# Kernel optimization log

Hardware: AMD Instinct MI355X
Metric: run time of the kernel (lower is better)

## Reference

```python
import jax, jax.numpy as jnp
import numpy as np
from jax import lax

INV_SQRT2 = np.float32(1.0 / np.sqrt(2.0))

def conv2d(x, w, b=None, stride=1, pad=0):
    y = lax.conv_general_dilated(x, w, (stride, stride), [(pad, pad), (pad, pad)],
                                 dimension_numbers=('NCHW', 'OIHW', 'NCHW'))
    return y if b is None else y + b[None, :, None, None]

def haar_dwt2_zero(x):
    # pytorch_wavelets DWTForward(J=1, wave='haar', mode='zero') for odd H,W:
    # pad one zero at the end of each spatial dim, then pairwise Haar analysis.
    x = jnp.pad(x, ((0, 0), (0, 0), (0, 1), (0, 1)))
    xe, xo = x[..., 0::2], x[..., 1::2]
    lo_w, hi_w = (xe + xo) * INV_SQRT2, (xe - xo) * INV_SQRT2
    def rows(t):
        te, to = t[:, :, 0::2, :], t[:, :, 1::2, :]
        return (te + to) * INV_SQRT2, (te - to) * INV_SQRT2
    ll, lh = rows(lo_w)
    hl, hh = rows(hi_w)
    return ll, lh, hl, hh  # cA, cH, cV, cD

def pixel_shuffle2(x):
    B, C, H, W = x.shape
    co = C // 4
    return x.reshape(B, co, 2, 2, H, W).transpose(0, 1, 4, 2, 5, 3).reshape(B, co, H * 2, W * 2)

def gaussian_kernel5(sigma=0.5):
    r = np.arange(5, dtype=np.float64) - 2.0
    k = np.exp(-(r ** 2) / (2.0 * sigma * sigma))
    return jnp.asarray((k / k.sum()).astype(np.float32))

_GK = gaussian_kernel5(0.5)

def gaussian_blur5(x4d):
    # cv2.GaussianBlur ksize=(5,5) sigma=0.5, default BORDER_REFLECT_101 -> 'reflect' pad
    p = jnp.pad(x4d, ((0, 0), (0, 0), (2, 2), (2, 2)), mode='reflect')
    p = conv2d(p, _GK.reshape(1, 1, 5, 1))
    return conv2d(p, _GK.reshape(1, 1, 1, 5))

def channel_attention(x, w1, w2):
    avg = jnp.mean(x, axis=(2, 3), keepdims=True)
    mx = jnp.max(x, axis=(2, 3), keepdims=True)
    mlp = lambda v: conv2d(jax.nn.relu(conv2d(v, w1)), w2)
    return jax.nn.sigmoid(mlp(avg) + mlp(mx)) * x

def _forward(x, w_x1, b_x1, w_x2, b_x2, w_x3, b_x3, w_hi, b_hi, w_lo, b_lo,
             ca1_w1, ca1_w2, ca2_w1, ca2_w2, w_cat, b_cat, w_c9a, b_c9a, w_c9b, b_c9b):
    f1 = jax.nn.relu(conv2d(x, w_x1, b_x1))            # (1,16,H,W)
    f2 = jax.nn.relu(conv2d(f1, w_x2, b_x2))           # (1,8,H,W)
    tmp12 = jax.nn.relu(conv2d(f2, w_x3, b_x3))        # (1,1,H,W)
    cA, cH, cV, cD = haar_dwt2_zero(tmp12)             # each (1,1,(H+1)/2,(W+1)/2)
    hf = pixel_shuffle2(jax.nn.relu(conv2d(jnp.concatenate([cH, cV, cD], 1), w_hi, b_hi, pad=1)))
    lf = pixel_shuffle2(jax.nn.relu(conv2d(cA, w_lo, b_lo, pad=1)))  # (1,1,H+5,W+5)
    # original detaches hf (cpu->numpy->cv2->cuda): gradients do not flow through it
    hf = gaussian_blur5(lax.stop_gradient(hf))
    hf = channel_attention(hf, ca1_w1, ca1_w2)
    lf = channel_attention(lf, ca2_w1, ca2_w2)
    alpha = 1.0
    cat = jax.nn.relu(conv2d(jnp.concatenate([alpha * hf, (1.0 - alpha) * lf], 1), w_cat, b_cat))
    f12 = tmp12 + cat                                   # (1,1,H,W)
    h = jax.nn.relu(conv2d(f12, w_c9a, b_c9a, pad=1))   # (1,32,H,W)
    return jax.nn.relu(conv2d(h, w_c9b, b_c9b, pad=1))  # (1,64,H,W)

def setup_inputs() -> dict:
    key = jax.random.key(0)
    ks = jax.random.split(key, 24)
    f32 = jnp.float32
    n = lambda k, s, sc=0.05: jax.random.normal(k, s, f32) * sc
    H = W = 511
    return {
        'x': jax.random.normal(ks[0], (1, 204, H, W), f32),
        'w_x1': n(ks[1], (16, 204, 1, 1)), 'b_x1': n(ks[2], (16,)),
        'w_x2': n(ks[3], (8, 16, 1, 1)),   'b_x2': n(ks[4], (8,)),
        'w_x3': n(ks[5], (1, 8, 1, 1)),    'b_x3': n(ks[6], (1,)),
        'w_hi': n(ks[7], (4, 3, 1, 1)),    'b_hi': n(ks[8], (4,)),
        'w_lo': n(ks[9], (4, 1, 1, 1)),    'b_lo': n(ks[10], (4,)),
        'ca1_w1': n(ks[11], (1, 1, 1, 1), 0.5), 'ca1_w2': n(ks[12], (1, 1, 1, 1), 0.5),
        'ca2_w1': n(ks[13], (1, 1, 1, 1), 0.5), 'ca2_w2': n(ks[14], (1, 1, 1, 1), 0.5),
        'w_cat': n(ks[15], (1, 2, 6, 6)),  'b_cat': n(ks[16], (1,)),
        'w_c9a': n(ks[17], (32, 1, 3, 3)), 'b_c9a': n(ks[18], (32,)),
        'w_c9b': n(ks[19], (64, 32, 3, 3)), 'b_c9b': n(ks[20], (64,)),
    }

def reference(x, w_x1, b_x1, w_x2, b_x2, w_x3, b_x3, w_hi, b_hi, w_lo, b_lo,
              ca1_w1, ca1_w2, ca2_w1, ca2_w2, w_cat, b_cat, w_c9a, b_c9a, w_c9b, b_c9b):
    return _forward(x, w_x1, b_x1, w_x2, b_x2, w_x3, b_x3, w_hi, b_hi, w_lo, b_lo,
                    ca1_w1, ca1_w2, ca2_w1, ca2_w2, w_cat, b_cat, w_c9a, b_c9a, w_c9b, b_c9b)
```

## Files before the change

### kernel.cpp

```cpp
#include <hip/hip_runtime.h>
#include <math.h>

#define NP    261121
#define HALF  130561
#define WPX   520
#define ROWN  4160
#define PSTR  2138240
#define NBLUR 1041

typedef __attribute__((ext_vector_type(8))) short short8;
typedef __attribute__((ext_vector_type(4))) float f32x4;

static __device__ __forceinline__ unsigned short f2bf(float f) {
    unsigned int u = __builtin_bit_cast(unsigned int, f);
    u += 0x7FFFu + ((u >> 16) & 1u);
    return (unsigned short)(u >> 16);
}

__global__ __launch_bounds__(256) void k_prep(const float* __restrict__ w_c9a,
                                              const float* __restrict__ w_c9b,
                                              const float* __restrict__ w_x1,
                                              float* __restrict__ wTa,
                                              unsigned short* __restrict__ wb2,
                                              float* __restrict__ wT1,
                                              unsigned short* __restrict__ h2)
{
    int t = blockIdx.x * 256 + threadIdx.x;
    if (t < 288)  wTa[t] = w_c9a[(t & 31) * 9 + (t >> 5)];
    if (t < 3264) wT1[t] = w_x1[(t & 15) * 204 + (t >> 4)];
    if (t < 18432) {
        int o = t / 288, ck = t - o * 288;
        int c = ck / 9, k = ck - c * 9;
        wb2[k * 2048 + o * 32 + c] = f2bf(w_c9b[t]);
    }
    short8 z8 = {0, 0, 0, 0, 0, 0, 0, 0};
    if (t < 4160) {
        int pl = t / 1040;
        int rr = t - pl * 1040;
        int row = rr >= 520 ? 512 : 0;
        int ch  = rr >= 520 ? rr - 520 : rr;
        *reinterpret_cast<short8*>(h2 + (size_t)pl * PSTR + (size_t)row * ROWN + ch * 8) = z8;
    }
    int z = t - 4160;
    if (z >= 0 && z < 6132) {
        int row = z / 12 + 1;
        int j = z - (row - 1) * 12;
        int pl = j / 3, cidx = j - pl * 3;
        int col = (cidx == 0) ? 0 : (cidx == 1 ? 512 : 513);
        *reinterpret_cast<short8*>(h2 + (size_t)pl * PSTR + (size_t)row * ROWN + col * 8) = z8;
    }
}

__global__ __launch_bounds__(512) void k_conv123(const float* __restrict__ x,
                                                 const float* __restrict__ wT1,
                                                 const float* __restrict__ b1,
                                                 const float* __restrict__ w2,
                                                 const float* __restrict__ b2,
                                                 const float* __restrict__ w3,
                                                 const float* __restrict__ b3,
                                                 float* __restrict__ tmp12)
{
    __shared__ float sw[3264];
    int t = threadIdx.x;
    for (int i = t; i < 3264; i += 512) sw[i] = wT1[i];
    __syncthreads();

    int g = blockIdx.x * 512 + t;
    if (g >= HALF) return;
    int p0 = g, p1 = g + HALF;
    bool has1 = p1 < NP;
    int p1c = has1 ? p1 : p0;

    float acc0[16], acc1[16];
#pragma unroll
    for (int o = 0; o < 16; ++o) { acc0[o] = 0.f; acc1[o] = 0.f; }

#pragma unroll 4
    for (int c = 0; c < 204; ++c) {
        float xv0 = x[c * NP + p0];
        float xv1 = x[c * NP + p1c];
        const float4* wv = reinterpret_cast<const float4*>(sw + c * 16);
        float wl[16];
        *reinterpret_cast<float4*>(&wl[0])  = wv[0];
        *reinterpret_cast<float4*>(&wl[4])  = wv[1];
        *reinterpret_cast<float4*>(&wl[8])  = wv[2];
        *reinterpret_cast<float4*>(&wl[12]) = wv[3];
#pragma unroll
        for (int o = 0; o < 16; ++o) {
            acc0[o] = fmaf(xv0, wl[o], acc0[o]);
            acc1[o] = fmaf(xv1, wl[o], acc1[o]);
        }
    }

    float r0 = b3[0], r1 = b3[0];
    {
        float f10[16], f11[16];
#pragma unroll
        for (int o = 0; o < 16; ++o) {
            float bo = b1[o];
            f10[o] = fmaxf(acc0[o] + bo, 0.f);
            f11[o] = fmaxf(acc1[o] + bo, 0.f);
        }
#pragma unroll
        for (int j = 0; j < 8; ++j) {
            float s0 = b2[j], s1 = b2[j];
#pragma unroll
            for (int o = 0; o < 16; ++o) {
                float w = w2[j * 16 + o];
                s0 = fmaf(f10[o], w, s0);
                s1 = fmaf(f11[o], w, s1);
            }
            float wj = w3[j];
            r0 = fmaf(fmaxf(s0, 0.f), wj, r0);
            r1 = fmaf(fmaxf(s1, 0.f), wj, r1);
        }
    }
    tmp12[p0] = fmaxf(r0, 0.f);
    if (has1) tmp12[p1] = fmaxf(r1, 0.f);
}

__global__ __launch_bounds__(256) void k_dwt_hi(const float* __restrict__ tmp12,
                                                const float* __restrict__ w_hi,
                                                const float* __restrict__ b_hi,
                                                float* __restrict__ hf)
{
    const float INV = 0.70710678118654752440f;
    int idx = blockIdx.x * 256 + threadIdx.x;
    if (idx >= 258 * 258) return;
    int h = idx / 258, w = idx - h * 258;

    float wh[12], bh[4];
#pragma unroll
    for (int i = 0; i < 12; ++i) wh[i] = w_hi[i];
#pragma unroll
    for (int o = 0; o < 4; ++o) bh[o] = b_hi[o];

    float v[4];
    if (h == 0 || h == 257 || w == 0 || w == 257) {
#pragma unroll
        for (int o = 0; o < 4; ++o) v[o] = fmaxf(bh[o], 0.f);
    } else {
        int hh = h - 1, ww = w - 1;
        int r0 = 2 * hh, r1 = 2 * hh + 1, c0 = 2 * ww, c1 = 2 * ww + 1;
        float a = tmp12[r0 * 511 + c0];
        float b = (c1 < 511) ? tmp12[r0 * 511 + c1] : 0.f;
        float c = (r1 < 511) ? tmp12[r1 * 511 + c0] : 0.f;
        float d = (r1 < 511 && c1 < 511) ? tmp12[r1 * 511 + c1] : 0.f;
        float lo0 = (a + b) * INV, hi0 = (a - b) * INV;
        float lo1 = (c + d) * INV, hi1 = (c - d) * INV;
        float cH = (lo0 - lo1) * INV;
        float cV = (hi0 + hi1) * INV;
        float cD = (hi0 - hi1) * INV;
#pragma unroll
        for (int o = 0; o < 4; ++o)
            v[o] = fmaxf(wh[o * 3 + 0] * cH + wh[o * 3 + 1] * cV + wh[o * 3 + 2] * cD + bh[o], 0.f);
    }
    int orow = (2 * h) * 516 + 2 * w;
    hf[orow]       = v[0];
    hf[orow + 1]   = v[1];
    hf[orow + 516] = v[2];
    hf[orow + 517] = v[3];
}

__global__ __launch_bounds__(256) void k_blur(const float* __restrict__ hf,
                                              float* __restrict__ hfb,
                                              float* __restrict__ psum,
                                              float* __restrict__ pmax,
                                              float g0, float g1, float g2)
{
    __shared__ float ss[256], sm[256];
    int t = threadIdx.x;
    int idx = blockIdx.x * 256 + t;
    bool ok = idx < 516 * 516;
    int idc = ok ? idx : 0;
    int y = idc / 516, x = idc - y * 516;
    float g[5] = {g0, g1, g2, g1, g0};
    int ry[5], rx[5];
#pragma unroll
    for (int i = 0; i < 5; ++i) {
        int yy = y + i - 2; yy = yy < 0 ? -yy : (yy > 515 ? 1030 - yy : yy);
        int xx = x + i - 2; xx = xx < 0 ? -xx : (xx > 515 ? 1030 - xx : xx);
        ry[i] = yy * 516; rx[i] = xx;
    }
    float s = 0.f;
#pragma unroll
    for (int i = 0; i < 5; ++i) {
        float rs = 0.f;
#pragma unroll
        for (int j = 0; j < 5; ++j) rs = fmaf(g[j], hf[ry[i] + rx[j]], rs);
        s = fmaf(g[i], rs, s);
    }
    if (ok) hfb[idx] = s;

    ss[t] = ok ? s : 0.f;
    sm[t] = ok ? s : -3.4e38f;
    __syncthreads();
    for (int off = 128; off > 0; off >>= 1) {
        if (t < off) { ss[t] += ss[t + off]; sm[t] = fmaxf(sm[t], sm[t + off]); }
        __syncthreads();
    }
    if (t == 0) { psum[blockIdx.x] = ss[0]; pmax[blockIdx.x] = sm[0]; }
}

__global__ __launch_bounds__(256) void k_cat(const float* __restrict__ hfb,
                                             const float* __restrict__ tmp12,
                                             const float* __restrict__ psum,
                                             const float* __restrict__ pmax,
                                             const float* __restrict__ caw1,
                                             const float* __restrict__ caw2,
                                             const float* __restrict__ w_cat,
                                             const float* __restrict__ b_cat,
                                             float* __restrict__ f12)
{
    __shared__ float ss[256], sm[256], ssc;
    int t = threadIdx.x;
    {
        float s = 0.f, m = -3.4e38f;
        for (int i = t; i < NBLUR; i += 256) { s += psum[i]; m = fmaxf(m, pmax[i]); }
        ss[t] = s; sm[t] = m;
        __syncthreads();
        for (int off = 128; off > 0; off >>= 1) {
            if (t < off) { ss[t] += ss[t + off]; sm[t] = fmaxf(sm[t], sm[t + off]); }
            __syncthreads();
        }
        if (t == 0) {
            float avg = ss[0] / 266256.f;
            float a = caw1[0], b = caw2[0];
            float z = b * fmaxf(a * avg, 0.f) + b * fmaxf(a * sm[0], 0.f);
            ssc = 1.f / (1.f + expf(-z));
        }
        __syncthreads();
    }
    float sc = ssc;

    int p = blockIdx.x * 256 + t;
    if (p >= NP) return;
    int y = p / 511, x = p - y * 511;
    float s = 0.f;
#pragma unroll
    for (int ky = 0; ky < 6; ++ky) {
        const float* row = hfb + (y + ky) * 516 + x;
#pragma unroll
        for (int kx = 0; kx < 6; ++kx) s = fmaf(row[kx], w_cat[ky * 6 + kx], s);
    }
    f12[p] = tmp12[p] + fmaxf(sc * s + b_cat[0], 0.f);
}

__global__ __launch_bounds__(256) void k_c9a(const float* __restrict__ f12,
                                             const float* __restrict__ wTa,
                                             const float* __restrict__ bias,
                                             unsigned short* __restrict__ h2)
{
    int p = blockIdx.x * 256 + threadIdx.x;
    if (p >= NP) return;
    int y = p / 511, x = p - y * 511;
    float hv[9];
#pragma unroll
    for (int ky = 0; ky < 3; ++ky)
#pragma unroll
        for (int kx = 0; kx < 3; ++kx) {
            int yy = y + ky - 1, xx = x + kx - 1;
            hv[ky * 3 + kx] = (yy >= 0 && yy < 511 && xx >= 0 && xx < 511) ? f12[yy * 511 + xx] : 0.f;
        }
    float acc[32];
#pragma unroll
    for (int o = 0; o < 32; ++o) acc[o] = bias[o];
#pragma unroll
    for (int k = 0; k < 9; ++k) {
        float v = hv[k];
        const float* wp = wTa + k * 32;
#pragma unroll
        for (int o = 0; o < 32; ++o) acc[o] = fmaf(v, wp[o], acc[o]);
    }
    unsigned short o16[32];
#pragma unroll
    for (int o = 0; o < 32; ++o) o16[o] = f2bf(fmaxf(acc[o], 0.f));
    size_t px = (size_t)(y + 1) * WPX + (x + 1);
#pragma unroll
    for (int i = 0; i < 4; ++i)
        *reinterpret_cast<short8*>(h2 + (size_t)i * PSTR + px * 8) =
            reinterpret_cast<const short8*>(o16)[i];
}

__global__ __launch_bounds__(256, 3) void k_c9b(const unsigned short* __restrict__ h2,
                                                const unsigned short* __restrict__ wb2,
                                                const float* __restrict__ bias,
                                                float* __restrict__ out)
{
    __shared__ unsigned short swu[9 * 2048];

    int bid = blockIdx.x;
    int xcd = bid & 7, jj = bid >> 3;
    const int q = 127, r = 6;
    int wg = (xcd < r ? xcd * (q + 1) : r * (q + 1) + (xcd - r) * q) + jj;

    int lane = threadIdx.x & 63;
    int wave = threadIdx.x >> 6;
    int y  = wg >> 1;
    int xh = wg & 1;
    int xb = xh * 256 + wave * 64;
    int lpx = lane & 15, kg = lane >> 4;

    {
        const short8* wsrc = reinterpret_cast<const short8*>(wb2);
        short8* wdst = reinterpret_cast<short8*>(swu);
        for (int d = threadIdx.x; d < 2304; d += 256) {
            int kt = d >> 8, rem = d & 255, m = rem >> 6, l = rem & 63;
            wdst[d] = wsrc[kt * 256 + (m * 16 + (l & 15)) * 4 + (l >> 4)];
        }
    }
    __syncthreads();

    f32x4 acc[4][4];
#pragma unroll
    for (int m = 0; m < 4; ++m)
#pragma unroll
        for (int n = 0; n < 4; ++n) acc[m][n] = (f32x4){0.f, 0.f, 0.f, 0.f};

    const unsigned short* hb = h2 + (size_t)kg * PSTR;
    const int base_px = (y + 1) * WPX + (xb + 1) + lpx;
    const int rowm = base_px - WPX, row0 = base_px, rowp = base_px + WPX;
    const short8* swv = reinterpret_cast<const short8*>(swu);

#define LOADB(BUF, ROW, DX) do { \
        const unsigned short* rp = hb + (size_t)((ROW) + (DX)) * 8; \
        BUF[0] = *reinterpret_cast<const short8*>(rp); \
        BUF[1] = *reinterpret_cast<const short8*>(rp + 128); \
        BUF[2] = *reinterpret_cast<const short8*>(rp + 256); \
        BUF[3] = *reinterpret_cast<const short8*>(rp + 384); \
    } while (0)

#define TAP(KT, BUF) do { \
        const short8* ap = swv + (KT) * 256 + lane; \
        short8 a0 = ap[0], a1 = ap[64], a2 = ap[128], a3 = ap[192]; \
        _Pragma("unroll") \
        for (int n = 0; n < 4; ++n) { \
            acc[0][n] = __builtin_amdgcn_mfma_f32_16x16x32_bf16(a0, BUF[n], acc[0][n], 0, 0, 0); \
            acc[1][n] = __builtin_amdgcn_mfma_f32_16x16x32_bf16(a1, BUF[n], acc[1][n], 0, 0, 0); \
            acc[2][n] = __builtin_amdgcn_mfma_f32_16x16x32_bf16(a2, BUF[n], acc[2][n], 0, 0, 0); \
            acc[3][n] = __builtin_amdgcn_mfma_f32_16x16x32_bf16(a3, BUF[n], acc[3][n], 0, 0, 0); \
        } \
    } while (0)

    short8 bX[4], bY[4], bZ[4];
    LOADB(bX, rowm, -1);
    LOADB(bY, rowm,  0);
    LOADB(bZ, rowm, +1); TAP(0, bX);
    LOADB(bX, row0, -1); TAP(1, bY);
    LOADB(bY, row0,  0); TAP(2, bZ);
    LOADB(bZ, row0, +1); TAP(3, bX);
    LOADB(bX, rowp, -1); TAP(4, bY);
    LOADB(bY, rowp,  0); TAP(5, bZ);
    LOADB(bZ, rowp, +1); TAP(6, bX);
    TAP(7, bY);
    TAP(8, bZ);
#undef LOADB
#undef TAP

    const int ybase = y * 511;
#pragma unroll
    for (int m = 0; m < 4; ++m) {
#pragma unroll
        for (int rr = 0; rr < 4; ++rr) {
            int o = m * 16 + kg * 4 + rr;
            float bo = bias[o];
#pragma unroll
            for (int n = 0; n < 4; ++n) {
                int px = xb + n * 16 + lpx;
                if (px < 511)
                    out[(size_t)o * NP + ybase + px] = fmaxf(acc[m][n][rr] + bo, 0.f);
            }
        }
    }
}

extern "C" void kernel_launch(void* const* d_in, const int* in_sizes, int n_in,
                              void* d_out, int out_size, void* d_ws, size_t ws_size,
                              hipStream_t stream)
{
    (void)in_sizes; (void)n_in; (void)out_size; (void)ws_size;

    const float* x     = (const float*)d_in[0];
    const float* w_x1  = (const float*)d_in[1];
    const float* b_x1  = (const float*)d_in[2];
    const float* w_x2  = (const float*)d_in[3];
    const float* b_x2  = (const float*)d_in[4];
    const float* w_x3  = (const float*)d_in[5];
    const float* b_x3  = (const float*)d_in[6];
    const float* w_hi  = (const float*)d_in[7];
    const float* b_hi  = (const float*)d_in[8];
    const float* ca1w1 = (const float*)d_in[11];
    const float* ca1w2 = (const float*)d_in[12];
    const float* w_cat = (const float*)d_in[15];
    const float* b_cat = (const float*)d_in[16];
    const float* w_c9a = (const float*)d_in[17];
    const float* b_c9a = (const float*)d_in[18];
    const float* w_c9b = (const float*)d_in[19];
    const float* b_c9b = (const float*)d_in[20];

    float* ws    = (float*)d_ws;
    float* tmp12 = ws + 0;
    float* hf    = ws + 261184;
    float* hfb   = ws + 527488;
    float* f12   = ws + 793792;
    float* psum  = ws + 1054976;
    float* pmax  = ws + 1056032;
    float* wTa   = ws + 1057088;
    float* wT1   = ws + 1057408;
    unsigned short* wb2 = (unsigned short*)(ws + 1060736);
    unsigned short* h2  = (unsigned short*)(ws + 1069952);

    float* out = (float*)d_out;

    double kk[5], ssum = 0.0;
    for (int i = 0; i < 5; ++i) { double r = i - 2.0; kk[i] = exp(-r * r / 0.5); ssum += kk[i]; }
    float g0 = (float)(kk[0] / ssum), g1 = (float)(kk[1] / ssum), g2 = (float)(kk[2] / ssum);

    k_prep<<<72, 256, 0, stream>>>(w_c9a, w_c9b, w_x1, wTa, wb2, wT1, h2);
    k_conv123<<<256, 512, 0, stream>>>(x, wT1, b_x1, w_x2, b_x2, w_x3, b_x3, tmp12);
    k_dwt_hi<<<261, 256, 0, stream>>>(tmp12, w_hi, b_hi, hf);
    k_blur<<<NBLUR, 256, 0, stream>>>(hf, hfb, psum, pmax, g0, g1, g2);
    k_cat<<<1021, 256, 0, stream>>>(hfb, tmp12, psum, pmax, ca1w1, ca1w2, w_cat, b_cat, f12);
    k_c9a<<<1021, 256, 0, stream>>>(f12, wTa, b_c9a, h2);
    k_c9b<<<1022, 256, 0, stream>>>(h2, wb2, b_c9b, out);
}
```

Measured before the change: 115.1 us.

## Remove prep kernel, fold weight prep into conv and DWT, four pixels per thread

Drops the separate k_prep launch. The w_x1 transpose now happens directly into shared memory inside k_conv123. The c9b bf16 weight packing and h2 border zeroing move into the DWT kernel, and k_c9a reads the untransposed w_c9a directly. k_conv123 now runs 256-thread blocks that each handle four pixels per thread instead of two, which raises register pressure and cuts the number of active threads to about 65K for a 261K-pixel conv over 204 channels. The goal is to save one launch and raise per-thread ILP, at the risk of lower occupancy in the dominant memory-bound conv.

```diff
diff --git a/kernel.cpp b/kernel.cpp
--- a/kernel.cpp
+++ b/kernel.cpp
@@ -2,7 +2,7 @@
 #include <math.h>
 
 #define NP    261121
-#define HALF  130561
+#define NQ    65281
 #define WPX   520
 #define ROWN  4160
 #define PSTR  2138240
@@ -17,17 +17,90 @@
     return (unsigned short)(u >> 16);
 }
 
-__global__ __launch_bounds__(256) void k_prep(const float* __restrict__ w_c9a,
-                                              const float* __restrict__ w_c9b,
-                                              const float* __restrict__ w_x1,
-                                              float* __restrict__ wTa,
-                                              unsigned short* __restrict__ wb2,
-                                              float* __restrict__ wT1,
-                                              unsigned short* __restrict__ h2)
+static __device__ __forceinline__ float finish_px(const float* __restrict__ acc,
+                                                  const float* __restrict__ b1,
+                                                  const float* __restrict__ w2,
+                                                  const float* __restrict__ b2,
+                                                  const float* __restrict__ w3,
+                                                  float b3v)
+{
+    float f1[16];
+#pragma unroll
+    for (int o = 0; o < 16; ++o) f1[o] = fmaxf(acc[o] + b1[o], 0.f);
+    float tmp = b3v;
+#pragma unroll
+    for (int j = 0; j < 8; ++j) {
+        float s = b2[j];
+#pragma unroll
+        for (int o = 0; o < 16; ++o) s = fmaf(f1[o], w2[j * 16 + o], s);
+        tmp = fmaf(fmaxf(s, 0.f), w3[j], tmp);
+    }
+    return fmaxf(tmp, 0.f);
+}
+
+__global__ __launch_bounds__(256) void k_conv123(const float* __restrict__ x,
+                                                 const float* __restrict__ w_x1,
+                                                 const float* __restrict__ b1,
+                                                 const float* __restrict__ w2,
+                                                 const float* __restrict__ b2,
+                                                 const float* __restrict__ w3,
+                                                 const float* __restrict__ b3,
+                                                 float* __restrict__ tmp12)
+{
+    __shared__ float sw[3264];
+    int t = threadIdx.x;
+    for (int i = t; i < 3264; i += 256) sw[i] = w_x1[(i & 15) * 204 + (i >> 4)];
+    __syncthreads();
+
+    int g = blockIdx.x * 256 + t;
+    if (g >= NQ) return;
+    int p0 = g, p1 = g + NQ, p2 = g + 2 * NQ, p3 = g + 3 * NQ;
+    bool has3 = p3 < NP;
+    int p3c = has3 ? p3 : p0;
+
+    float a0[16], a1[16], a2[16], a3[16];
+#pragma unroll
+    for (int o = 0; o < 16; ++o) { a0[o] = 0.f; a1[o] = 0.f; a2[o] = 0.f; a3[o] = 0.f; }
+
+#pragma unroll 4
+    for (int c = 0; c < 204; ++c) {
+        int off = c * NP;
+        float x0 = x[off + p0];
+        float x1 = x[off + p1];
+        float x2 = x[off + p2];
+        float x3 = x[off + p3c];
+        const float4* wv = reinterpret_cast<const float4*>(sw + c * 16);
+        float wl[16];
+        *reinterpret_cast<float4*>(&wl[0])  = wv[0];
+        *reinterpret_cast<float4*>(&wl[4])  = wv[1];
+        *reinterpret_cast<float4*>(&wl[8])  = wv[2];
+        *reinterpret_cast<float4*>(&wl[12]) = wv[3];
+#pragma unroll
+        for (int o = 0; o < 16; ++o) {
+            a0[o] = fmaf(x0, wl[o], a0[o]);
+            a1[o] = fmaf(x1, wl[o], a1[o]);
+            a2[o] = fmaf(x2, wl[o], a2[o]);
+            a3[o] = fmaf(x3, wl[o], a3[o]);
+        }
+    }
+
+    float b3v = b3[0];
+    tmp12[p0] = finish_px(a0, b1, w2, b2, w3, b3v);
+    tmp12[p1] = finish_px(a1, b1, w2, b2, w3, b3v);
+    tmp12[p2] = finish_px(a2, b1, w2, b2, w3, b3v);
+    if (has3) tmp12[p3] = finish_px(a3, b1, w2, b2, w3, b3v);
+}
+
+__global__ __launch_bounds__(256) void k_dwt(const float* __restrict__ tmp12,
+                                             const float* __restrict__ w_hi,
+                                             const float* __restrict__ b_hi,
+                                             const float* __restrict__ w_c9b,
+                                             float* __restrict__ hf,
+                                             unsigned short* __restrict__ wb2,
+                                             unsigned short* __restrict__ h2)
 {
     int t = blockIdx.x * 256 + threadIdx.x;
-    if (t < 288)  wTa[t] = w_c9a[(t & 31) * 9 + (t >> 5)];
-    if (t < 3264) wT1[t] = w_x1[(t & 15) * 204 + (t >> 4)];
+
     if (t < 18432) {
         int o = t / 288, ck = t - o * 288;
         int c = ck / 9, k = ck - c * 9;
@@ -49,85 +122,10 @@
         int col = (cidx == 0) ? 0 : (cidx == 1 ? 512 : 513);
         *reinterpret_cast<short8*>(h2 + (size_t)pl * PSTR + (size_t)row * ROWN + col * 8) = z8;
     }
-}
-
-__global__ __launch_bounds__(512) void k_conv123(const float* __restrict__ x,
-                                                 const float* __restrict__ wT1,
-                                                 const float* __restrict__ b1,
-                                                 const float* __restrict__ w2,
-                                                 const float* __restrict__ b2,
-                                                 const float* __restrict__ w3,
-                                                 const float* __restrict__ b3,
-                                                 float* __restrict__ tmp12)
-{
-    __shared__ float sw[3264];
-    int t = threadIdx.x;
-    for (int i = t; i < 3264; i += 512) sw[i] = wT1[i];
-    __syncthreads();
-
-    int g = blockIdx.x * 512 + t;
-    if (g >= HALF) return;
-    int p0 = g, p1 = g + HALF;
-    bool has1 = p1 < NP;
-    int p1c = has1 ? p1 : p0;
-
-    float acc0[16], acc1[16];
-#pragma unroll
-    for (int o = 0; o < 16; ++o) { acc0[o] = 0.f; acc1[o] = 0.f; }
-
-#pragma unroll 4
-    for (int c = 0; c < 204; ++c) {
-        float xv0 = x[c * NP + p0];
-        float xv1 = x[c * NP + p1c];
-        const float4* wv = reinterpret_cast<const float4*>(sw + c * 16);
-        float wl[16];
-        *reinterpret_cast<float4*>(&wl[0])  = wv[0];
-        *reinterpret_cast<float4*>(&wl[4])  = wv[1];
-        *reinterpret_cast<float4*>(&wl[8])  = wv[2];
-        *reinterpret_cast<float4*>(&wl[12]) = wv[3];
-#pragma unroll
-        for (int o = 0; o < 16; ++o) {
-            acc0[o] = fmaf(xv0, wl[o], acc0[o]);
-            acc1[o] = fmaf(xv1, wl[o], acc1[o]);
-        }
-    }
-
-    float r0 = b3[0], r1 = b3[0];
-    {
-        float f10[16], f11[16];
-#pragma unroll
-        for (int o = 0; o < 16; ++o) {
-            float bo = b1[o];
-            f10[o] = fmaxf(acc0[o] + bo, 0.f);
-            f11[o] = fmaxf(acc1[o] + bo, 0.f);
-        }
-#pragma unroll
-        for (int j = 0; j < 8; ++j) {
-            float s0 = b2[j], s1 = b2[j];
-#pragma unroll
-            for (int o = 0; o < 16; ++o) {
-                float w = w2[j * 16 + o];
-                s0 = fmaf(f10[o], w, s0);
-                s1 = fmaf(f11[o], w, s1);
-            }
-            float wj = w3[j];
-            r0 = fmaf(fmaxf(s0, 0.f), wj, r0);
-            r1 = fmaf(fmaxf(s1, 0.f), wj, r1);
-        }
-    }
-    tmp12[p0] = fmaxf(r0, 0.f);
-    if (has1) tmp12[p1] = fmaxf(r1, 0.f);
-}
-
-__global__ __launch_bounds__(256) void k_dwt_hi(const float* __restrict__ tmp12,
-                                                const float* __restrict__ w_hi,
-                                                const float* __restrict__ b_hi,
-                                                float* __restrict__ hf)
-{
+
     const float INV = 0.70710678118654752440f;
-    int idx = blockIdx.x * 256 + threadIdx.x;
-    if (idx >= 258 * 258) return;
-    int h = idx / 258, w = idx - h * 258;
+    if (t >= 258 * 258) return;
+    int h = t / 258, w = t - h * 258;
 
     float wh[12], bh[4];
 #pragma unroll
@@ -247,7 +245,7 @@
 }
 
 __global__ __launch_bounds__(256) void k_c9a(const float* __restrict__ f12,
-                                             const float* __restrict__ wTa,
+                                             const float* __restrict__ w_c9a,
                                              const float* __restrict__ bias,
                                              unsigned short* __restrict__ h2)
 {
@@ -268,9 +266,8 @@
 #pragma unroll
     for (int k = 0; k < 9; ++k) {
         float v = hv[k];
-        const float* wp = wTa + k * 32;
-#pragma unroll
-        for (int o = 0; o < 32; ++o) acc[o] = fmaf(v, wp[o], acc[o]);
+#pragma unroll
+        for (int o = 0; o < 32; ++o) acc[o] = fmaf(v, w_c9a[o * 9 + k], acc[o]);
     }
     unsigned short o16[32];
 #pragma unroll
@@ -405,10 +402,8 @@
     float* f12   = ws + 793792;
     float* psum  = ws + 1054976;
     float* pmax  = ws + 1056032;
-    float* wTa   = ws + 1057088;
-    float* wT1   = ws + 1057408;
-    unsigned short* wb2 = (unsigned short*)(ws + 1060736);
-    unsigned short* h2  = (unsigned short*)(ws + 1069952);
+    unsigned short* wb2 = (unsigned short*)(ws + 1057088);
+    unsigned short* h2  = (unsigned short*)(ws + 1066304);
 
     float* out = (float*)d_out;
 
@@ -416,11 +411,10 @@
     for (int i = 0; i < 5; ++i) { double r = i - 2.0; kk[i] = exp(-r * r / 0.5); ssum += kk[i]; }
     float g0 = (float)(kk[0] / ssum), g1 = (float)(kk[1] / ssum), g2 = (float)(kk[2] / ssum);
 
-    k_prep<<<72, 256, 0, stream>>>(w_c9a, w_c9b, w_x1, wTa, wb2, wT1, h2);
-    k_conv123<<<256, 512, 0, stream>>>(x, wT1, b_x1, w_x2, b_x2, w_x3, b_x3, tmp12);
-    k_dwt_hi<<<261, 256, 0, stream>>>(tmp12, w_hi, b_hi, hf);
+    k_conv123<<<256, 256, 0, stream>>>(x, w_x1, b_x1, w_x2, b_x2, w_x3, b_x3, tmp12);
+    k_dwt<<<261, 256, 0, stream>>>(tmp12, w_hi, b_hi, w_c9b, hf, wb2, h2);
     k_blur<<<NBLUR, 256, 0, stream>>>(hf, hfb, psum, pmax, g0, g1, g2);
     k_cat<<<1021, 256, 0, stream>>>(hfb, tmp12, psum, pmax, ca1w1, ca1w2, w_cat, b_cat, f12);
-    k_c9a<<<1021, 256, 0, stream>>>(f12, wTa, b_c9a, h2);
+    k_c9a<<<1021, 256, 0, stream>>>(f12, w_c9a, b_c9a, h2);
     k_c9b<<<1022, 256, 0, stream>>>(h2, wb2, b_c9b, out);
 }
```

Result: slower. 165.2 us (+43.6%).
